# Performance work log

Measured on AMD Instinct MI355X. Metric: run time of the kernel, lower is better.

The kernel has to match this reference:

```python
import jax, jax.numpy as jnp
import numpy as np

HEADS = 16
DIM_HEAD = 64
WINDOW = 128
LOOK_BACKWARD = 1
LOOK_FORWARD = 0
THETA = 10000.0
PAD_VALUE = -1


def look_around(x, backward, forward, pad_value, axis):
    """Gather overlapping windows: concat shifted copies along the intra-window axis."""
    w = x.shape[axis]
    size = backward + forward + 1
    pads = [(0, 0)] * x.ndim
    pads[axis] = (backward, forward)
    p = jnp.pad(x, pads, constant_values=pad_value)
    segs = [jax.lax.slice_in_dim(p, s, s + w, axis=axis) for s in range(size)]
    return jnp.concatenate(segs, axis=axis + 1)


def rotate_half(t):
    t1, t2 = jnp.split(t, 2, axis=-1)
    return jnp.concatenate([-t2, t1], axis=-1)


def setup_inputs() -> dict:
    key = jax.random.key(0)
    k1, k2, k3 = jax.random.split(key, 3)
    dim = 1024
    x = jax.random.normal(k1, (4, 4096, dim), dtype=jnp.float32)
    W_qkv = jax.random.normal(k2, (dim, 3 * HEADS * DIM_HEAD), dtype=jnp.float32) * (dim ** -0.5)
    W_out = jax.random.normal(k3, (HEADS * DIM_HEAD, dim), dtype=jnp.float32) * ((HEADS * DIM_HEAD) ** -0.5)
    return {"x": x, "W_qkv": W_qkv, "W_out": W_out}


def reference(x, W_qkv, W_out):
    b, n, dim = x.shape
    h, dh, ws = HEADS, DIM_HEAD, WINDOW
    w = n // ws
    j = ws * (LOOK_BACKWARD + LOOK_FORWARD + 1)  # 256 keys per query window

    qkv = x @ W_qkv  # (b, n, 3*h*dh)
    q, k, v = jnp.split(qkv, 3, axis=-1)

    def to_bhwnd(t):
        return t.reshape(b, n, h, dh).transpose(0, 2, 1, 3).reshape(b, h, w, ws, dh)

    bq = to_bhwnd(q) * (dh ** -0.5)
    bk = look_around(to_bhwnd(k), LOOK_BACKWARD, LOOK_FORWARD, float(PAD_VALUE), axis=2)
    bv = look_around(to_bhwnd(v), LOOK_BACKWARD, LOOK_FORWARD, float(PAD_VALUE), axis=2)

    # rotary embeddings over the look-around key length; queries use last ws positions
    inv_freq = 1.0 / (THETA ** (jnp.arange(0, dh, 2, dtype=jnp.float32) / dh))
    t_pos = jnp.arange(j, dtype=jnp.float32)
    freqs = t_pos[:, None] * inv_freq[None, :]
    freqs = jnp.concatenate([freqs, freqs], axis=-1)  # (j, dh)
    q_freqs = freqs[-ws:]
    bq = bq * jnp.cos(q_freqs) + rotate_half(bq) * jnp.sin(q_freqs)
    bk = bk * jnp.cos(freqs) + rotate_half(bk) * jnp.sin(freqs)

    sim = jnp.einsum('bhwid,bhwjd->bhwij', bq, bk)  # (b,h,w,ws,j)

    seq = jnp.arange(n).reshape(w, ws)
    bq_t = seq[:, :, None]  # (w, ws, 1)
    bq_k = look_around(seq[None], LOOK_BACKWARD, LOOK_FORWARD, PAD_VALUE, axis=1)[0]  # (w, j)
    bq_k = bq_k[:, None, :]  # (w, 1, j)
    pad_mask = bq_k == PAD_VALUE
    # causal + exact window (look_backward * window_size)
    causal_mask = (bq_t < bq_k) | (bq_t > bq_k + ws * LOOK_BACKWARD)
    mask = causal_mask | pad_mask

    mask_value = -jnp.finfo(sim.dtype).max
    sim = jnp.where(mask, mask_value, sim)
    attn = jax.nn.softmax(sim, axis=-1)

    out = jnp.einsum('bhwij,bhwjd->bhwid', attn, bv)
    out = out.reshape(b, h, n, dh).transpose(0, 2, 1, 3).reshape(b, n, h * dh)
    return out @ W_out
```

## Files before the change

kernel.cpp:

```cpp
#include <hip/hip_runtime.h>
#include <stdint.h>


typedef __attribute__((ext_vector_type(8))) short bfrag;
typedef __attribute__((ext_vector_type(4))) float f4;

#define MFMA_BF16(a, b, c) __builtin_amdgcn_mfma_f32_16x16x32_bf16((a), (b), (c), 0, 0, 0)

static __device__ __forceinline__ short f2bf(float f) {
  unsigned u = __builtin_bit_cast(unsigned, f);
  u = (u + 0x7fffu + ((u >> 16) & 1u)) >> 16;
  return (short)u;
}
static __device__ __forceinline__ float bf2f(short s) {
  unsigned u = ((unsigned)(unsigned short)s) << 16;
  return __builtin_bit_cast(float, u);
}

typedef __attribute__((address_space(3))) unsigned lds_u;
typedef __attribute__((address_space(1))) unsigned gbl_u;

static __device__ __forceinline__ void gl_lds16(const void* g, const void* lds) {
  unsigned loff = (unsigned)__builtin_amdgcn_readfirstlane((int)(uintptr_t)lds);
  __builtin_amdgcn_global_load_lds((gbl_u*)(uintptr_t)g, (lds_u*)(uintptr_t)loff, 16, 0, 0);
}

__global__ __launch_bounds__(256) void convert_x(const float* __restrict__ x,
                                                 short* __restrict__ xb) {
  int idx = blockIdx.x * 256 + threadIdx.x;
  size_t base = (size_t)idx * 8;
  float4 a = *(const float4*)(x + base);
  float4 b = *(const float4*)(x + base + 4);
  bfrag o;
  o[0] = f2bf(a.x); o[1] = f2bf(a.y); o[2] = f2bf(a.z); o[3] = f2bf(a.w);
  o[4] = f2bf(b.x); o[5] = f2bf(b.y); o[6] = f2bf(b.z); o[7] = f2bf(b.w);
  *(bfrag*)(xb + base) = o;
}

__global__ __launch_bounds__(256) void transpose_w(
    const float* __restrict__ wqkv, const float* __restrict__ wout,
    short* __restrict__ wqkvT, short* __restrict__ woutT) {
  __shared__ short t[64][72];
  const int tid = threadIdx.x;
  const int kt = blockIdx.x, yt = blockIdx.y;
  const float* src; short* dst; int N, nt;
  if (yt < 48) { src = wqkv; dst = wqkvT; N = 3072; nt = yt; }
  else         { src = wout; dst = woutT; N = 1024; nt = yt - 48; }
  const int k0 = kt * 64, n0 = nt * 64;
#pragma unroll
  for (int i = 0; i < 4; ++i) {
    int r = i * 16 + (tid >> 4);
    int c = (tid & 15) * 4;
    float4 v = *(const float4*)(src + (size_t)(k0 + r) * N + n0 + c);
    t[c + 0][r] = f2bf(v.x);
    t[c + 1][r] = f2bf(v.y);
    t[c + 2][r] = f2bf(v.z);
    t[c + 3][r] = f2bf(v.w);
  }
  __syncthreads();
#pragma unroll
  for (int i = 0; i < 2; ++i) {
    int c = tid + i * 256;
    int n = c >> 3, k8 = (c & 7) * 8;
    *(bfrag*)(dst + (size_t)(n0 + n) * 1024 + k0 + k8) = *(const bfrag*)&t[n][k8];
  }
}

#define VM6 asm volatile("s_waitcnt vmcnt(6)" ::: "memory")
#define VM4 asm volatile("s_waitcnt vmcnt(4)" ::: "memory")
#define VM0 asm volatile("s_waitcnt vmcnt(0)" ::: "memory")
#define VNOP ((void)0)

#define ST_A(buf, ks, kk)                                                          \
  do {                                                                             \
    gl_lds16(aS0 + (ks) * 32 + (kk), ldsA + (buf) * 32768 + (ks) * 16384 + stA);   \
    gl_lds16(aS1 + (ks) * 32 + (kk),                                               \
             ldsA + (buf) * 32768 + (ks) * 16384 + 8192 + stA);                    \
  } while (0)
#define ST_B(buf, ks, kk)                                                          \
  do {                                                                             \
    gl_lds16(bS0 + (ks) * 32 + (kk), ldsB + (buf) * 32768 + (ks) * 16384 + stA);   \
    gl_lds16(bS1 + (ks) * 32 + (kk),                                               \
             ldsB + (buf) * 32768 + (ks) * 16384 + 8192 + stA);                    \
  } while (0)

#define MM4(mi, a)                                 \
  acc[mi][0] = MFMA_BF16(a, b0, acc[mi][0]);       \
  acc[mi][1] = MFMA_BF16(a, b1, acc[mi][1]);       \
  acc[mi][2] = MFMA_BF16(a, b2, acc[mi][2]);       \
  acc[mi][3] = MFMA_BF16(a, b3, acc[mi][3])

#define PHASE(buf, ks, mh, STAGE, WAIT)                                            \
  {                                                                                \
    const char* pA_ = ldsA + (buf) * 32768 + (ks) * 16384 + (mh) * 4096 + aRd;     \
    const char* pB_ = ldsB + (buf) * 32768 + (ks) * 16384 + bRd;                   \
    bfrag a0 = *(const bfrag*)(pA_);                                               \
    bfrag a1 = *(const bfrag*)(pA_ + 1024);                                        \
    bfrag a2 = *(const bfrag*)(pA_ + 2048);                                        \
    bfrag a3 = *(const bfrag*)(pA_ + 3072);                                        \
    bfrag b0 = *(const bfrag*)(pB_);                                               \
    bfrag b1 = *(const bfrag*)(pB_ + 1024);                                        \
    bfrag b2 = *(const bfrag*)(pB_ + 2048);                                        \
    bfrag b3 = *(const bfrag*)(pB_ + 3072);                                        \
    STAGE;                                                                         \
    WAIT;                                                                          \
    __builtin_amdgcn_s_barrier();                                                  \
    asm volatile("s_waitcnt lgkmcnt(0)" ::: "memory");                             \
    __builtin_amdgcn_sched_barrier(0);                                             \
    __builtin_amdgcn_s_setprio(1);                                                 \
    MM4((mh) * 4 + 0, a0);                                                         \
    MM4((mh) * 4 + 1, a1);                                                         \
    MM4((mh) * 4 + 2, a2);                                                         \
    MM4((mh) * 4 + 3, a3);                                                         \
    __builtin_amdgcn_s_setprio(0);                                                 \
  }

template <int MODE, int NBX>
__global__ __launch_bounds__(512, 2) void gemm256(
    const short* __restrict__ A, const short* __restrict__ Bt, float* __restrict__ C,
    short* __restrict__ oq, short* __restrict__ ok, short* __restrict__ ov) {
  __shared__ __align__(1024) char lds[131072];
  char* const ldsA = lds;
  char* const ldsB = lds + 65536;

  const int tid = threadIdx.x, lane = tid & 63, wv = tid >> 6;
  const int wr = wv >> 2, wc = wv & 3;
  const int l15 = lane & 15, quad = lane >> 4;

  const int nwg = NBX * 64;
  const int bid = (int)blockIdx.x;
  const int wgid = (bid & 7) * (nwg >> 3) + (bid >> 3);
  const int bx = wgid % NBX, by = wgid / NBX;

  const short* Ab = A + (size_t)by * 256 * 1024;
  const short* Bb = Bt + (size_t)bx * 256 * 1024;

  const int srow = lane & 15, scg = lane >> 4;
  const short* aS0 = Ab + (size_t)(wv * 16 + srow) * 1024 + scg * 8;
  const short* aS1 = Ab + (size_t)((8 + wv) * 16 + srow) * 1024 + scg * 8;
  const short* bS0 = Bb + (size_t)(wv * 16 + srow) * 1024 + scg * 8;
  const short* bS1 = Bb + (size_t)((8 + wv) * 16 + srow) * 1024 + scg * 8;
  const int stA = wv * 1024;

  const int rdoff = lane * 16;
  const int aRd = wr * 8192 + rdoff;
  const int bRd = wc * 4096 + rdoff;

  f4 acc[8][4];
#pragma unroll
  for (int i = 0; i < 8; ++i)
#pragma unroll
    for (int j = 0; j < 4; ++j) acc[i][j] = (f4)0.f;

  ST_A(0, 0, 0); ST_B(0, 0, 0); ST_A(0, 1, 0); ST_B(0, 1, 0); ST_A(1, 0, 64);
  VM6;
  __builtin_amdgcn_s_barrier();

#pragma unroll 1
  for (int t = 0; t < 14; t += 2) {
    const int kk1 = t * 64 + 64, kk2 = t * 64 + 128, kk3 = t * 64 + 192;
    PHASE(0, 0, 0, ST_B(1, 0, kk1), VNOP);
    PHASE(0, 0, 1, ST_A(1, 1, kk1), VM6);
    PHASE(0, 1, 0, ST_B(1, 1, kk1), VNOP);
    PHASE(0, 1, 1, ST_A(0, 0, kk2), VM6);
    PHASE(1, 0, 0, ST_B(0, 0, kk2), VNOP);
    PHASE(1, 0, 1, ST_A(0, 1, kk2), VM6);
    PHASE(1, 1, 0, ST_B(0, 1, kk2), VNOP);
    PHASE(1, 1, 1, ST_A(1, 0, kk3), VM6);
  }

  PHASE(0, 0, 0, ST_B(1, 0, 960), VNOP);
  PHASE(0, 0, 1, ST_A(1, 1, 960), VM6);
  PHASE(0, 1, 0, ST_B(1, 1, 960), VNOP);
  PHASE(0, 1, 1, VNOP, VM4);
  PHASE(1, 0, 0, VNOP, VNOP);
  PHASE(1, 0, 1, VNOP, VM0);
  PHASE(1, 1, 0, VNOP, VNOP);
  PHASE(1, 1, 1, VNOP, VNOP);

  if constexpr (MODE == 0) {
    const int n64 = bx * 256 + wc * 64;
    const int part = n64 >> 10;
    const int head = (n64 & 1023) >> 6;
    short* o = (part == 0) ? oq : (part == 1) ? ok : ov;
    const float f0 = exp2f((float)l15 * -0.41524101186f);
    const float f1 = exp2f((float)(16 + l15) * -0.41524101186f);
#pragma unroll
    for (int i = 0; i < 8; ++i)
#pragma unroll
      for (int r = 0; r < 4; ++r) {
        const int m = by * 256 + wr * 128 + i * 16 + quad * 4 + r;
        const int b = m >> 12, p = m & 4095;
        short* row = o + ((size_t)(b * 16 + head) * 4096 + p) * 64;
        if (part == 2) {
#pragma unroll
          for (int j = 0; j < 4; ++j) row[j * 16 + l15] = f2bf(acc[i][j][r]);
        } else {
#pragma unroll
          for (int j = 0; j < 2; ++j) {
            float av = acc[i][j][r], bv2 = acc[i][j + 2][r];
            float sn, cs;
            __sincosf((float)p * (j ? f1 : f0), &sn, &cs);
            float ra = av * cs - bv2 * sn;
            float rb = bv2 * cs + av * sn;
            if (part == 0) { ra *= 0.125f; rb *= 0.125f; }
            row[j * 16 + l15] = f2bf(ra);
            row[32 + j * 16 + l15] = f2bf(rb);
          }
        }
      }
  } else {
#pragma unroll
    for (int i = 0; i < 8; ++i)
#pragma unroll
      for (int j = 0; j < 4; ++j)
#pragma unroll
        for (int r = 0; r < 4; ++r) {
          int m = by * 256 + wr * 128 + i * 16 + quad * 4 + r;
          int n = bx * 256 + wc * 64 + j * 16 + l15;
          C[(size_t)m * 1024 + n] = acc[i][j][r];
        }
  }
}

__global__ __launch_bounds__(256) void attn_kernel(
    const short* __restrict__ qb, const short* __restrict__ kb,
    const short* __restrict__ vb, short* __restrict__ ob) {
  constexpr int KST = 72, VST = 264, PST = 136;
  __shared__ __align__(16) short smem[18432 + 16896];
  short* Ks = smem;
  short* Pl = smem;
  short* Vt = smem + 18432;

  const int bid = blockIdx.x;
  const int w = bid & 31, bh = bid >> 5;
  const int tid = threadIdx.x, lane = tid & 63, wv = tid >> 6;
  const int l15 = lane & 15, quad = lane >> 4;
  const size_t kvbase = (size_t)bh * (4096 * 64);
  const int pk0 = w * 128 - 128;

  const int i0 = wv * 32;
  const short* qbase = qb + kvbase + (size_t)(w * 128) * 64;
  bfrag aq[2][2];
#pragma unroll
  for (int rt = 0; rt < 2; ++rt)
#pragma unroll
    for (int ks = 0; ks < 2; ++ks)
      aq[rt][ks] = *(const bfrag*)(qbase + (size_t)(i0 + rt * 16 + l15) * 64 + ks * 32 + quad * 8);

#pragma unroll
  for (int i = 0; i < 8; ++i) {
    int c = tid + i * 256;
    int row = c >> 3;
    int d0 = (c & 7) * 8;
    int pk = pk0 + row;
    if (pk < 0) pk = 0;
    const size_t src = kvbase + (size_t)pk * 64 + d0;
    bfrag kvv = *(const bfrag*)(kb + src);
    *(bfrag*)&Ks[row * KST + d0] = kvv;
    bfrag vvv = *(const bfrag*)(vb + src);
#pragma unroll
    for (int j = 0; j < 8; ++j) Vt[(d0 + j) * VST + row] = vvv[j];
  }
  __syncthreads();

  f4 sim[2][16];
#pragma unroll
  for (int rt = 0; rt < 2; ++rt)
#pragma unroll
    for (int ct = 0; ct < 16; ++ct) sim[rt][ct] = (f4)0.f;

#pragma unroll
  for (int ct = 0; ct < 16; ++ct) {
    bfrag bk0 = *(const bfrag*)&Ks[(ct * 16 + l15) * KST + quad * 8];
    bfrag bk1 = *(const bfrag*)&Ks[(ct * 16 + l15) * KST + 32 + quad * 8];
#pragma unroll
    for (int rt = 0; rt < 2; ++rt) {
      sim[rt][ct] = MFMA_BF16(aq[rt][0], bk0, sim[rt][ct]);
      sim[rt][ct] = MFMA_BF16(aq[rt][1], bk1, sim[rt][ct]);
    }
  }
  __syncthreads();

  float linv[2][4];
#pragma unroll
  for (int rt = 0; rt < 2; ++rt)
#pragma unroll
    for (int r = 0; r < 4; ++r) {
      const int iloc = i0 + rt * 16 + quad * 4 + r;
      float sum = 0.f;
#pragma unroll
      for (int ct = 0; ct < 16; ++ct) {
        int jj = ct * 16 + l15;
        bool valid = (jj >= iloc) && (jj <= iloc + 128) && ((w > 0) || (jj >= 128));
        float pv = valid ? __expf(sim[rt][ct][r]) : 0.f;
        sim[rt][ct][r] = pv;
        sum += pv;
      }
#pragma unroll
      for (int off = 1; off < 16; off <<= 1) sum += __shfl_xor(sum, off);
      linv[rt][r] = 1.f / sum;
    }

  f4 oacc[2][4];
#pragma unroll
  for (int rt = 0; rt < 2; ++rt)
#pragma unroll
    for (int ctd = 0; ctd < 4; ++ctd) oacc[rt][ctd] = (f4)0.f;

#pragma unroll
  for (int pass = 0; pass < 2; ++pass) {
#pragma unroll
    for (int rt = 0; rt < 2; ++rt)
#pragma unroll
      for (int ct = 0; ct < 8; ++ct) {
        int ctg = pass * 8 + ct;
#pragma unroll
        for (int r = 0; r < 4; ++r)
          Pl[(i0 + rt * 16 + quad * 4 + r) * PST + ct * 16 + l15] = f2bf(sim[rt][ctg][r]);
      }
#pragma unroll
    for (int ks = 0; ks < 4; ++ks) {
      bfrag ap[2];
#pragma unroll
      for (int rt = 0; rt < 2; ++rt)
        ap[rt] = *(const bfrag*)&Pl[(i0 + rt * 16 + l15) * PST + ks * 32 + quad * 8];
#pragma unroll
      for (int ctd = 0; ctd < 4; ++ctd) {
        bfrag bv = *(const bfrag*)&Vt[(ctd * 16 + l15) * VST + pass * 128 + ks * 32 + quad * 8];
#pragma unroll
        for (int rt = 0; rt < 2; ++rt) oacc[rt][ctd] = MFMA_BF16(ap[rt], bv, oacc[rt][ctd]);
      }
    }
  }

  const int b = bh >> 4, h = bh & 15;
  short* obase = ob + ((size_t)b * 4096 + w * 128) * 1024 + h * 64;
#pragma unroll
  for (int rt = 0; rt < 2; ++rt)
#pragma unroll
    for (int ctd = 0; ctd < 4; ++ctd)
#pragma unroll
      for (int r = 0; r < 4; ++r) {
        int i = i0 + rt * 16 + quad * 4 + r;
        int d = ctd * 16 + l15;
        obase[(size_t)i * 1024 + d] = f2bf(oacc[rt][ctd][r] * linv[rt][r]);
      }
}

extern "C" void kernel_launch(void* const* d_in, const int* in_sizes, int n_in,
                              void* d_out, int out_size, void* d_ws, size_t ws_size,
                              hipStream_t stream) {
  const float* x = (const float*)d_in[0];
  const float* wqkv = (const float*)d_in[1];
  const float* wout = (const float*)d_in[2];
  float* out = (float*)d_out;
  char* ws = (char*)d_ws;

  short* qb = (short*)(ws + 0);
  short* kb = (short*)(ws + 33554432);
  short* vb = (short*)(ws + 67108864);
  short* xb = (short*)(ws + 100663296);
  short* ab = xb;
  short* wqkvT = (short*)(ws + 134217728);
  short* woutT = (short*)(ws + 140509184);

  convert_x<<<8192, 256, 0, stream>>>(x, xb);
  transpose_w<<<dim3(16, 64), 256, 0, stream>>>(wqkv, wout, wqkvT, woutT);
  gemm256<0, 12><<<768, 512, 0, stream>>>(xb, wqkvT, nullptr, qb, kb, vb);
  attn_kernel<<<2048, 256, 0, stream>>>(qb, kb, vb, ab);
  gemm256<1, 4><<<256, 512, 0, stream>>>(ab, woutT, out, nullptr, nullptr, nullptr);
}
```

Measured before the change: 357.4 us.

## Merge GEMM half-phases into full k-step phases and use rotation recurrence for RoPE

The GEMM main loop now handles a full 256-row k-slice per phase, loading all eight A fragments and issuing 32 MFMAs between barriers. This halves the number of barriers and waits per k-step and stages A and B for a slice together, at the cost of more live registers and a shallower prefetch distance. The QKV epilogue replaces the per-element sincos with an angle-addition recurrence that advances cos/sin by one position per row and by 13 positions between 16-row blocks. Repeated rotation updates can accumulate small floating-point error compared with computing each angle directly.

```diff
diff --git a/kernel.cpp b/kernel.cpp
--- a/kernel.cpp
+++ b/kernel.cpp
@@ -66,7 +66,6 @@
   }
 }
 
-#define VM6 asm volatile("s_waitcnt vmcnt(6)" ::: "memory")
 #define VM4 asm volatile("s_waitcnt vmcnt(4)" ::: "memory")
 #define VM0 asm volatile("s_waitcnt vmcnt(0)" ::: "memory")
 #define VNOP ((void)0)
@@ -83,6 +82,7 @@
     gl_lds16(bS1 + (ks) * 32 + (kk),                                               \
              ldsB + (buf) * 32768 + (ks) * 16384 + 8192 + stA);                    \
   } while (0)
+#define ST2(buf, ks, kk) do { ST_A(buf, ks, kk); ST_B(buf, ks, kk); } while (0)
 
 #define MM4(mi, a)                                 \
   acc[mi][0] = MFMA_BF16(a, b0, acc[mi][0]);       \
@@ -90,14 +90,18 @@
   acc[mi][2] = MFMA_BF16(a, b2, acc[mi][2]);       \
   acc[mi][3] = MFMA_BF16(a, b3, acc[mi][3])
 
-#define PHASE(buf, ks, mh, STAGE, WAIT)                                            \
+#define PHASE2(buf, ks, STAGE, WAIT)                                               \
   {                                                                                \
-    const char* pA_ = ldsA + (buf) * 32768 + (ks) * 16384 + (mh) * 4096 + aRd;     \
+    const char* pA_ = ldsA + (buf) * 32768 + (ks) * 16384 + aRd;                   \
     const char* pB_ = ldsB + (buf) * 32768 + (ks) * 16384 + bRd;                   \
     bfrag a0 = *(const bfrag*)(pA_);                                               \
     bfrag a1 = *(const bfrag*)(pA_ + 1024);                                        \
     bfrag a2 = *(const bfrag*)(pA_ + 2048);                                        \
     bfrag a3 = *(const bfrag*)(pA_ + 3072);                                        \
+    bfrag a4 = *(const bfrag*)(pA_ + 4096);                                        \
+    bfrag a5 = *(const bfrag*)(pA_ + 5120);                                        \
+    bfrag a6 = *(const bfrag*)(pA_ + 6144);                                        \
+    bfrag a7 = *(const bfrag*)(pA_ + 7168);                                        \
     bfrag b0 = *(const bfrag*)(pB_);                                               \
     bfrag b1 = *(const bfrag*)(pB_ + 1024);                                        \
     bfrag b2 = *(const bfrag*)(pB_ + 2048);                                        \
@@ -108,10 +112,14 @@
     asm volatile("s_waitcnt lgkmcnt(0)" ::: "memory");                             \
     __builtin_amdgcn_sched_barrier(0);                                             \
     __builtin_amdgcn_s_setprio(1);                                                 \
-    MM4((mh) * 4 + 0, a0);                                                         \
-    MM4((mh) * 4 + 1, a1);                                                         \
-    MM4((mh) * 4 + 2, a2);                                                         \
-    MM4((mh) * 4 + 3, a3);                                                         \
+    MM4(0, a0);                                                                    \
+    MM4(1, a1);                                                                    \
+    MM4(2, a2);                                                                    \
+    MM4(3, a3);                                                                    \
+    MM4(4, a4);                                                                    \
+    MM4(5, a5);                                                                    \
+    MM4(6, a6);                                                                    \
+    MM4(7, a7);                                                                    \
     __builtin_amdgcn_s_setprio(0);                                                 \
   }
 
@@ -142,9 +150,8 @@
   const short* bS1 = Bb + (size_t)((8 + wv) * 16 + srow) * 1024 + scg * 8;
   const int stA = wv * 1024;
 
-  const int rdoff = lane * 16;
-  const int aRd = wr * 8192 + rdoff;
-  const int bRd = wc * 4096 + rdoff;
+  const int aRd = wr * 8192 + lane * 16;
+  const int bRd = wc * 4096 + lane * 16;
 
   f4 acc[8][4];
 #pragma unroll
@@ -152,63 +159,83 @@
 #pragma unroll
     for (int j = 0; j < 4; ++j) acc[i][j] = (f4)0.f;
 
-  ST_A(0, 0, 0); ST_B(0, 0, 0); ST_A(0, 1, 0); ST_B(0, 1, 0); ST_A(1, 0, 64);
-  VM6;
+  ST2(0, 0, 0); ST2(0, 1, 0);
+  VM4;
   __builtin_amdgcn_s_barrier();
 
 #pragma unroll 1
   for (int t = 0; t < 14; t += 2) {
-    const int kk1 = t * 64 + 64, kk2 = t * 64 + 128, kk3 = t * 64 + 192;
-    PHASE(0, 0, 0, ST_B(1, 0, kk1), VNOP);
-    PHASE(0, 0, 1, ST_A(1, 1, kk1), VM6);
-    PHASE(0, 1, 0, ST_B(1, 1, kk1), VNOP);
-    PHASE(0, 1, 1, ST_A(0, 0, kk2), VM6);
-    PHASE(1, 0, 0, ST_B(0, 0, kk2), VNOP);
-    PHASE(1, 0, 1, ST_A(0, 1, kk2), VM6);
-    PHASE(1, 1, 0, ST_B(0, 1, kk2), VNOP);
-    PHASE(1, 1, 1, ST_A(1, 0, kk3), VM6);
-  }
-
-  PHASE(0, 0, 0, ST_B(1, 0, 960), VNOP);
-  PHASE(0, 0, 1, ST_A(1, 1, 960), VM6);
-  PHASE(0, 1, 0, ST_B(1, 1, 960), VNOP);
-  PHASE(0, 1, 1, VNOP, VM4);
-  PHASE(1, 0, 0, VNOP, VNOP);
-  PHASE(1, 0, 1, VNOP, VM0);
-  PHASE(1, 1, 0, VNOP, VNOP);
-  PHASE(1, 1, 1, VNOP, VNOP);
+    const int kn = t * 64 + 64, kn2 = t * 64 + 128;
+    PHASE2(0, 0, ST2(1, 0, kn), VM4);
+    PHASE2(0, 1, ST2(1, 1, kn), VM4);
+    PHASE2(1, 0, ST2(0, 0, kn2), VM4);
+    PHASE2(1, 1, ST2(0, 1, kn2), VM4);
+  }
+
+  PHASE2(0, 0, ST2(1, 0, 960), VM4);
+  PHASE2(0, 1, ST2(1, 1, 960), VM4);
+  PHASE2(1, 0, VNOP, VM0);
+  PHASE2(1, 1, VNOP, VNOP);
 
   if constexpr (MODE == 0) {
     const int n64 = bx * 256 + wc * 64;
     const int part = n64 >> 10;
     const int head = (n64 & 1023) >> 6;
     short* o = (part == 0) ? oq : (part == 1) ? ok : ov;
-    const float f0 = exp2f((float)l15 * -0.41524101186f);
-    const float f1 = exp2f((float)(16 + l15) * -0.41524101186f);
-#pragma unroll
-    for (int i = 0; i < 8; ++i)
-#pragma unroll
-      for (int r = 0; r < 4; ++r) {
-        const int m = by * 256 + wr * 128 + i * 16 + quad * 4 + r;
-        const int b = m >> 12, p = m & 4095;
-        short* row = o + ((size_t)(b * 16 + head) * 4096 + p) * 64;
-        if (part == 2) {
+    const int mbase = by * 256 + wr * 128;
+    const int bb = mbase >> 12;
+    const int p0 = (mbase & 4095) + quad * 4;
+    short* const obase = o + (size_t)(bb * 16 + head) * 4096 * 64;
+    if (part == 2) {
+#pragma unroll
+      for (int i = 0; i < 8; ++i)
+#pragma unroll
+        for (int r = 0; r < 4; ++r) {
+          short* row = obase + (size_t)(p0 + i * 16 + r) * 64;
 #pragma unroll
           for (int j = 0; j < 4; ++j) row[j * 16 + l15] = f2bf(acc[i][j][r]);
-        } else {
+        }
+    } else {
+      const float qs = (part == 0) ? 0.125f : 1.0f;
+      float fr[2], c1[2], s1[2], cD[2], sD[2], cs[2], sn[2];
+      fr[0] = exp2f((float)l15 * -0.41524101186f);
+      fr[1] = exp2f((float)(16 + l15) * -0.41524101186f);
+#pragma unroll
+      for (int j = 0; j < 2; ++j) {
+        __sincosf(fr[j], &s1[j], &c1[j]);
+        __sincosf(13.0f * fr[j], &sD[j], &cD[j]);
+        __sincosf((float)p0 * fr[j], &sn[j], &cs[j]);
+      }
+#pragma unroll
+      for (int i = 0; i < 8; ++i) {
+#pragma unroll
+        for (int r = 0; r < 4; ++r) {
+          short* row = obase + (size_t)(p0 + i * 16 + r) * 64;
 #pragma unroll
           for (int j = 0; j < 2; ++j) {
             float av = acc[i][j][r], bv2 = acc[i][j + 2][r];
-            float sn, cs;
-            __sincosf((float)p * (j ? f1 : f0), &sn, &cs);
-            float ra = av * cs - bv2 * sn;
-            float rb = bv2 * cs + av * sn;
-            if (part == 0) { ra *= 0.125f; rb *= 0.125f; }
+            float ra = (av * cs[j] - bv2 * sn[j]) * qs;
+            float rb = (bv2 * cs[j] + av * sn[j]) * qs;
             row[j * 16 + l15] = f2bf(ra);
             row[32 + j * 16 + l15] = f2bf(rb);
           }
+          if (r < 3) {
+#pragma unroll
+            for (int j = 0; j < 2; ++j) {
+              float nc = cs[j] * c1[j] - sn[j] * s1[j];
+              sn[j] = sn[j] * c1[j] + cs[j] * s1[j];
+              cs[j] = nc;
+            }
+          }
         }
-      }
+#pragma unroll
+        for (int j = 0; j < 2; ++j) {
+          float nc = cs[j] * cD[j] - sn[j] * sD[j];
+          sn[j] = sn[j] * cD[j] + cs[j] * sD[j];
+          cs[j] = nc;
+        }
+      }
+    }
   } else {
 #pragma unroll
     for (int i = 0; i < 8; ++i)
```

Result: no change. 356.0 us (-0.4%).
